# Kernel optimization log

Hardware: AMD Instinct MI355X
Metric: run time of the kernel (lower is better)

The kernel has to match this reference:

```python
import jax, jax.numpy as jnp
import numpy as np

NEG_SLOPE = 0.1  # LeakyReLU alpha from __init__
EPS = 1e-5


def setup_inputs() -> dict:
    key = jax.random.key(0)
    k1, k2, k3, k4, k5 = jax.random.split(key, 5)
    N, E, DIN, DOUT = 10000, 160000, 1024, 1024
    x = jax.random.normal(k1, (N, DIN), dtype=jnp.float32)
    W = jax.random.normal(k2, (DIN, DOUT), dtype=jnp.float32) * 0.02  # xavier-ish gain
    a = jax.random.normal(k3, (1, 2 * DOUT), dtype=jnp.float32) * 0.02
    src = jax.random.randint(k4, (E,), 0, N, dtype=jnp.int64)  # edge rows i
    dst = jax.random.randint(k5, (E,), 0, N, dtype=jnp.int64)  # edge cols j
    return {"x": x, "W": W, "a": a, "src": src, "dst": dst}


def reference(x, W, a, src, dst):
    N = x.shape[0]
    d = W.shape[1]
    h = x @ W                                   # [N, d]
    # a @ cat(h_src, h_dst)^T == (h @ a_l)[src] + (h @ a_r)[dst]
    a_l, a_r = a[0, :d], a[0, d:]
    al = h @ a_l                                # [N]
    ar = h @ a_r                                # [N]
    e = jnp.exp(-jax.nn.leaky_relu(al[src] + ar[dst], negative_slope=NEG_SLOPE))  # [E]
    # sparse rowsum: A @ ones  ->  segment_sum of e over rows
    rowsum = jax.ops.segment_sum(e, src, num_segments=N)          # [N]
    # sparse aggregate: A @ h  (dropout = identity in eval mode)
    h_prime = jax.ops.segment_sum(e[:, None] * h[dst], src, num_segments=N)  # [N, d]
    h_prime = h_prime / (rowsum[:, None] + EPS)
    return jax.nn.elu(h_prime)  # concat=True branch
```

## Files before the change

kernel.cpp:

```cpp
#include <hip/hip_runtime.h>
#include <hip/hip_bf16.h>
#include <stdint.h>
#include <math.h>

#define DK 1024
#define DN 1024
#define CAP 64

typedef __attribute__((ext_vector_type(8))) short bf16x8;
typedef __attribute__((ext_vector_type(4))) float f32x4;

__device__ __forceinline__ unsigned short f2bf(float f) {
  union { float f; uint32_t u; } v; v.f = f;
  uint32_t r = v.u + 0x7FFFu + ((v.u >> 16) & 1u);
  return (unsigned short)(r >> 16);
}
__device__ __forceinline__ float bf2f(unsigned short b) {
  union { uint32_t u; float f; } v; v.u = ((uint32_t)b) << 16; return v.f;
}

__device__ __forceinline__ void gload_lds16(const void* g, void* l) {
  __builtin_amdgcn_global_load_lds((const __attribute__((address_space(1))) unsigned int*)g,
                                   (__attribute__((address_space(3))) unsigned int*)l,
                                   16, 0, 0);
}

__global__ __launch_bounds__(256) void prep_kernel(const float* __restrict__ x,
                                                   unsigned short* __restrict__ xb,
                                                   const float* __restrict__ W,
                                                   unsigned short* __restrict__ Wt,
                                                   int nchunks, int nCast) {
  if ((int)blockIdx.x < nCast) {
    int i = blockIdx.x * 256 + threadIdx.x;
    if (i < nchunks) {
      float4 v = ((const float4*)x)[i];
      ushort4 o;
      o.x = f2bf(v.x); o.y = f2bf(v.y); o.z = f2bf(v.z); o.w = f2bf(v.w);
      ((ushort4*)xb)[i] = o;
    }
  } else {
    __shared__ float t[32][33];
    int bid = blockIdx.x - nCast;
    int tx = threadIdx.x & 31, ty = threadIdx.x >> 5;
    int bk = (bid & 31) * 32, bn = (bid >> 5) * 32;
#pragma unroll
    for (int rr = 0; rr < 4; ++rr) {
      int row = ty + rr * 8;
      t[row][tx] = W[(size_t)(bk + row) * DN + bn + tx];
    }
    __syncthreads();
#pragma unroll
    for (int rr = 0; rr < 4; ++rr) {
      int row = ty + rr * 8;
      Wt[(size_t)(bn + row) * DK + bk + tx] = f2bf(t[tx][row]);
    }
  }
}

__global__ __launch_bounds__(256) void gemm_kernel(const unsigned short* __restrict__ A,
                                                   const unsigned short* __restrict__ Bt,
                                                   unsigned short* __restrict__ Hb,
                                                   int M) {
  __shared__ unsigned short As[128 * 32];
  __shared__ unsigned short Bs[128 * 32];
  const int tid = threadIdx.x;
  const int w = tid >> 6, lane = tid & 63;
  const int r = lane & 15, q = lane >> 4;
  const int m0 = blockIdx.x * 128, n0 = blockIdx.y * 128;
  const int wr = (w >> 1) * 64, wc = (w & 1) * 64;

  const int c0 = w * 64 + lane;
  const int rowA0 = c0 >> 2, g0 = c0 & 3;
  const int rowA1 = rowA0 + 64;
  int gr0 = m0 + rowA0; if (gr0 >= M) gr0 = M - 1;
  int gr1 = m0 + rowA1; if (gr1 >= M) gr1 = M - 1;
  const unsigned short* gA0 = A + (size_t)gr0 * DK + g0 * 8;
  const unsigned short* gA1 = A + (size_t)gr1 * DK + g0 * 8;
  const unsigned short* gB0 = Bt + (size_t)(n0 + rowA0) * DK + g0 * 8;
  const unsigned short* gB1 = Bt + (size_t)(n0 + rowA1) * DK + g0 * 8;
  unsigned short* lA0 = As + w * 512;
  unsigned short* lA1 = As + 2048 + w * 512;
  unsigned short* lB0 = Bs + w * 512;
  unsigned short* lB1 = Bs + 2048 + w * 512;

  const f32x4 zero = {0.f, 0.f, 0.f, 0.f};
  f32x4 acc[4][4];
#pragma unroll
  for (int i = 0; i < 4; ++i)
#pragma unroll
    for (int j = 0; j < 4; ++j) acc[i][j] = zero;

  for (int k0 = 0; k0 < DK; k0 += 32) {
    gload_lds16(gA0, lA0);
    gload_lds16(gA1, lA1);
    gload_lds16(gB0, lB0);
    gload_lds16(gB1, lB1);
    gA0 += 32; gA1 += 32; gB0 += 32; gB1 += 32;
    __syncthreads();

    bf16x8 af[4], bfr[4];
#pragma unroll
    for (int i = 0; i < 4; ++i)
      af[i] = *(const bf16x8*)&As[(wr + i * 16 + r) * 32 + q * 8];
#pragma unroll
    for (int j = 0; j < 4; ++j)
      bfr[j] = *(const bf16x8*)&Bs[(wc + j * 16 + r) * 32 + q * 8];
#pragma unroll
    for (int i = 0; i < 4; ++i)
#pragma unroll
      for (int j = 0; j < 4; ++j)
        acc[i][j] = __builtin_amdgcn_mfma_f32_16x16x32_bf16(af[i], bfr[j], acc[i][j], 0, 0, 0);
    __syncthreads();
  }

#pragma unroll
  for (int i = 0; i < 4; ++i) {
#pragma unroll
    for (int reg = 0; reg < 4; ++reg) {
      int m = m0 + wr + i * 16 + q * 4 + reg;
      if (m < M) {
#pragma unroll
        for (int j = 0; j < 4; ++j) {
          int n = n0 + wc + j * 16 + r;
          Hb[(size_t)m * DN + n] = f2bf(acc[i][j][reg]);
        }
      }
    }
  }
}

__global__ __launch_bounds__(256) void alar_kernel(const unsigned short* __restrict__ Hb,
                                                   const float* __restrict__ a,
                                                   float* __restrict__ al,
                                                   float* __restrict__ ar,
                                                   int M) {
  int row = blockIdx.x;
  int tid = threadIdx.x;
  ushort4 hv = ((const ushort4*)(Hb + (size_t)row * DN))[tid];
  float4 l4 = ((const float4*)a)[tid];
  float4 r4 = ((const float4*)(a + DN))[tid];
  float h0 = bf2f(hv.x), h1 = bf2f(hv.y), h2 = bf2f(hv.z), h3 = bf2f(hv.w);
  float pl = h0 * l4.x + h1 * l4.y + h2 * l4.z + h3 * l4.w;
  float pr = h0 * r4.x + h1 * r4.y + h2 * r4.z + h3 * r4.w;
#pragma unroll
  for (int off = 32; off >= 1; off >>= 1) {
    pl += __shfl_down(pl, off);
    pr += __shfl_down(pr, off);
  }
  __shared__ float sl[4], sr[4];
  int w = tid >> 6, lane = tid & 63;
  if (lane == 0) { sl[w] = pl; sr[w] = pr; }
  __syncthreads();
  if (tid == 0) {
    al[row] = sl[0] + sl[1] + sl[2] + sl[3];
    ar[row] = sr[0] + sr[1] + sr[2] + sr[3];
  }
}

__global__ __launch_bounds__(256) void edge_kernel(const int* __restrict__ src,
                                                   const int* __restrict__ dst,
                                                   const float* __restrict__ al,
                                                   const float* __restrict__ ar,
                                                   int* __restrict__ cnt,
                                                   int* __restrict__ bdst,
                                                   float* __restrict__ be, int E) {
  int i = blockIdx.x * 256 + threadIdx.x;
  if (i < E) {
    int s = src[i], d = dst[i];
    float v = al[s] + ar[d];
    float lr = v > 0.f ? v : 0.1f * v;
    float e = expf(-lr);
    int pos = atomicAdd(&cnt[s], 1);
    if (pos < CAP) {
      bdst[(s << 6) + pos] = d;
      be[(s << 6) + pos] = e;
    }
  }
}

__global__ __launch_bounds__(256) void aggregate_kernel(const int* __restrict__ cnt,
                                                        const int* __restrict__ bdst,
                                                        const float* __restrict__ be,
                                                        const unsigned short* __restrict__ Hb,
                                                        float* __restrict__ out, int M) {
  int row = blockIdx.x;
  int tid = threadIdx.x;
  int n = cnt[row]; if (n > CAP) n = CAP;
  int base = row << 6;
  size_t coff = (size_t)tid * 4;
  float a0 = 0.f, a1 = 0.f, a2 = 0.f, a3 = 0.f, rs = 0.f;
  int p = 0;
  for (; p + 8 <= n; p += 8) {
    int4 da = *(const int4*)(bdst + base + p);
    int4 db = *(const int4*)(bdst + base + p + 4);
    float4 ea = *(const float4*)(be + base + p);
    float4 eb = *(const float4*)(be + base + p + 4);
    ushort4 h0 = *(const ushort4*)&Hb[(size_t)da.x * DN + coff];
    ushort4 h1 = *(const ushort4*)&Hb[(size_t)da.y * DN + coff];
    ushort4 h2 = *(const ushort4*)&Hb[(size_t)da.z * DN + coff];
    ushort4 h3 = *(const ushort4*)&Hb[(size_t)da.w * DN + coff];
    ushort4 h4 = *(const ushort4*)&Hb[(size_t)db.x * DN + coff];
    ushort4 h5 = *(const ushort4*)&Hb[(size_t)db.y * DN + coff];
    ushort4 h6 = *(const ushort4*)&Hb[(size_t)db.z * DN + coff];
    ushort4 h7 = *(const ushort4*)&Hb[(size_t)db.w * DN + coff];
    rs += ((ea.x + ea.y) + (ea.z + ea.w)) + ((eb.x + eb.y) + (eb.z + eb.w));
    a0 += ea.x * bf2f(h0.x) + ea.y * bf2f(h1.x) + ea.z * bf2f(h2.x) + ea.w * bf2f(h3.x)
        + eb.x * bf2f(h4.x) + eb.y * bf2f(h5.x) + eb.z * bf2f(h6.x) + eb.w * bf2f(h7.x);
    a1 += ea.x * bf2f(h0.y) + ea.y * bf2f(h1.y) + ea.z * bf2f(h2.y) + ea.w * bf2f(h3.y)
        + eb.x * bf2f(h4.y) + eb.y * bf2f(h5.y) + eb.z * bf2f(h6.y) + eb.w * bf2f(h7.y);
    a2 += ea.x * bf2f(h0.z) + ea.y * bf2f(h1.z) + ea.z * bf2f(h2.z) + ea.w * bf2f(h3.z)
        + eb.x * bf2f(h4.z) + eb.y * bf2f(h5.z) + eb.z * bf2f(h6.z) + eb.w * bf2f(h7.z);
    a3 += ea.x * bf2f(h0.w) + ea.y * bf2f(h1.w) + ea.z * bf2f(h2.w) + ea.w * bf2f(h3.w)
        + eb.x * bf2f(h4.w) + eb.y * bf2f(h5.w) + eb.z * bf2f(h6.w) + eb.w * bf2f(h7.w);
  }
  for (; p + 4 <= n; p += 4) {
    int4 d4 = *(const int4*)(bdst + base + p);
    float4 e4 = *(const float4*)(be + base + p);
    ushort4 h0 = *(const ushort4*)&Hb[(size_t)d4.x * DN + coff];
    ushort4 h1 = *(const ushort4*)&Hb[(size_t)d4.y * DN + coff];
    ushort4 h2 = *(const ushort4*)&Hb[(size_t)d4.z * DN + coff];
    ushort4 h3 = *(const ushort4*)&Hb[(size_t)d4.w * DN + coff];
    rs += (e4.x + e4.y) + (e4.z + e4.w);
    a0 += e4.x * bf2f(h0.x) + e4.y * bf2f(h1.x) + e4.z * bf2f(h2.x) + e4.w * bf2f(h3.x);
    a1 += e4.x * bf2f(h0.y) + e4.y * bf2f(h1.y) + e4.z * bf2f(h2.y) + e4.w * bf2f(h3.y);
    a2 += e4.x * bf2f(h0.z) + e4.y * bf2f(h1.z) + e4.z * bf2f(h2.z) + e4.w * bf2f(h3.z);
    a3 += e4.x * bf2f(h0.w) + e4.y * bf2f(h1.w) + e4.z * bf2f(h2.w) + e4.w * bf2f(h3.w);
  }
  for (; p < n; ++p) {
    int d = bdst[base + p];
    float e = be[base + p];
    rs += e;
    ushort4 hv = *(const ushort4*)&Hb[(size_t)d * DN + coff];
    a0 += e * bf2f(hv.x);
    a1 += e * bf2f(hv.y);
    a2 += e * bf2f(hv.z);
    a3 += e * bf2f(hv.w);
  }
  float inv = 1.f / (rs + 1e-5f);
  float4 o; float v;
  v = a0 * inv; o.x = v > 0.f ? v : (expf(v) - 1.f);
  v = a1 * inv; o.y = v > 0.f ? v : (expf(v) - 1.f);
  v = a2 * inv; o.z = v > 0.f ? v : (expf(v) - 1.f);
  v = a3 * inv; o.w = v > 0.f ? v : (expf(v) - 1.f);
  ((float4*)(out + (size_t)row * DN))[tid] = o;
}

extern "C" void kernel_launch(void* const* d_in, const int* in_sizes, int n_in,
                              void* d_out, int out_size, void* d_ws, size_t ws_size,
                              hipStream_t stream) {
  const float* x = (const float*)d_in[0];
  const float* W = (const float*)d_in[1];
  const float* a = (const float*)d_in[2];
  const int* src = (const int*)d_in[3];
  const int* dst = (const int*)d_in[4];
  float* out = (float*)d_out;
  const int M = in_sizes[0] / DK;
  const int E = in_sizes[3];

  size_t off = 0;
  auto alloc = [&](size_t bytes) -> void* {
    void* p = (char*)d_ws + off;
    off += (bytes + 255) & ~(size_t)255;
    return p;
  };
  unsigned short* xb   = (unsigned short*)alloc((size_t)M * DK * 2);
  unsigned short* Wt   = (unsigned short*)alloc((size_t)DK * DN * 2);
  unsigned short* Hb   = (unsigned short*)alloc((size_t)M * DN * 2);
  float*          al   = (float*)alloc((size_t)M * 4);
  float*          ar   = (float*)alloc((size_t)M * 4);
  int*            cnt  = (int*)alloc((size_t)M * 4);
  int*            bdst = (int*)alloc((size_t)M * CAP * 4);
  float*          be   = (float*)alloc((size_t)M * CAP * 4);

  hipMemsetAsync(cnt, 0, (size_t)M * 4, stream);

  int nchunks = M * DK / 4;
  int nCast = (nchunks + 255) / 256;
  prep_kernel<<<nCast + (DK / 32) * (DN / 32), 256, 0, stream>>>(x, xb, W, Wt, nchunks, nCast);
  gemm_kernel<<<dim3((M + 127) / 128, DN / 128), 256, 0, stream>>>(xb, Wt, Hb, M);
  alar_kernel<<<M, 256, 0, stream>>>(Hb, a, al, ar, M);
  edge_kernel<<<(E + 255) / 256, 256, 0, stream>>>(src, dst, al, ar, cnt, bdst, be, E);
  aggregate_kernel<<<M, 256, 0, stream>>>(cnt, bdst, be, Hb, out, M);
}
```

Baseline: 201.5 us.

## Compute attention logits via precomputed W·a vectors fused into cast kernel

Result: faster. 194.7 us (-3.4%).

```diff
diff --git a/kernel.cpp b/kernel.cpp
--- a/kernel.cpp
+++ b/kernel.cpp
@@ -25,22 +25,65 @@
                                    16, 0, 0);
 }
 
+__device__ __forceinline__ void block_reduce2(float& pl, float& pr) {
+#pragma unroll
+  for (int off = 32; off >= 1; off >>= 1) {
+    pl += __shfl_down(pl, off);
+    pr += __shfl_down(pr, off);
+  }
+  __shared__ float sl[4], sr[4];
+  int w = threadIdx.x >> 6, lane = threadIdx.x & 63;
+  if (lane == 0) { sl[w] = pl; sr[w] = pr; }
+  __syncthreads();
+  if (threadIdx.x == 0) {
+    pl = sl[0] + sl[1] + sl[2] + sl[3];
+    pr = sr[0] + sr[1] + sr[2] + sr[3];
+  }
+}
+
+__global__ __launch_bounds__(256) void wvec_kernel(const float* __restrict__ W,
+                                                   const float* __restrict__ a,
+                                                   float* __restrict__ wl,
+                                                   float* __restrict__ wr,
+                                                   int* __restrict__ cnt, int M) {
+  int idx = blockIdx.x * 256 + threadIdx.x;
+  if (idx < M) cnt[idx] = 0;
+  int k = blockIdx.x;
+  int tid = threadIdx.x;
+  float4 wv = ((const float4*)(W + (size_t)k * DN))[tid];
+  float4 l4 = ((const float4*)a)[tid];
+  float4 r4 = ((const float4*)(a + DN))[tid];
+  float pl = wv.x * l4.x + wv.y * l4.y + wv.z * l4.z + wv.w * l4.w;
+  float pr = wv.x * r4.x + wv.y * r4.y + wv.z * r4.z + wv.w * r4.w;
+  block_reduce2(pl, pr);
+  if (tid == 0) { wl[k] = pl; wr[k] = pr; }
+}
+
 __global__ __launch_bounds__(256) void prep_kernel(const float* __restrict__ x,
                                                    unsigned short* __restrict__ xb,
                                                    const float* __restrict__ W,
                                                    unsigned short* __restrict__ Wt,
-                                                   int nchunks, int nCast) {
-  if ((int)blockIdx.x < nCast) {
-    int i = blockIdx.x * 256 + threadIdx.x;
-    if (i < nchunks) {
-      float4 v = ((const float4*)x)[i];
-      ushort4 o;
-      o.x = f2bf(v.x); o.y = f2bf(v.y); o.z = f2bf(v.z); o.w = f2bf(v.w);
-      ((ushort4*)xb)[i] = o;
-    }
+                                                   const float* __restrict__ wl,
+                                                   const float* __restrict__ wr,
+                                                   float* __restrict__ al,
+                                                   float* __restrict__ ar,
+                                                   int M) {
+  if ((int)blockIdx.x < M) {
+    int row = blockIdx.x;
+    int tid = threadIdx.x;
+    float4 v = ((const float4*)(x + (size_t)row * DK))[tid];
+    ushort4 o;
+    o.x = f2bf(v.x); o.y = f2bf(v.y); o.z = f2bf(v.z); o.w = f2bf(v.w);
+    ((ushort4*)(xb + (size_t)row * DK))[tid] = o;
+    float4 l4 = ((const float4*)wl)[tid];
+    float4 r4 = ((const float4*)wr)[tid];
+    float pl = v.x * l4.x + v.y * l4.y + v.z * l4.z + v.w * l4.w;
+    float pr = v.x * r4.x + v.y * r4.y + v.z * r4.z + v.w * r4.w;
+    block_reduce2(pl, pr);
+    if (tid == 0) { al[row] = pl; ar[row] = pr; }
   } else {
     __shared__ float t[32][33];
-    int bid = blockIdx.x - nCast;
+    int bid = blockIdx.x - M;
     int tx = threadIdx.x & 31, ty = threadIdx.x >> 5;
     int bk = (bid & 31) * 32, bn = (bid >> 5) * 32;
 #pragma unroll
@@ -126,34 +169,6 @@
         }
       }
     }
-  }
-}
-
-__global__ __launch_bounds__(256) void alar_kernel(const unsigned short* __restrict__ Hb,
-                                                   const float* __restrict__ a,
-                                                   float* __restrict__ al,
-                                                   float* __restrict__ ar,
-                                                   int M) {
-  int row = blockIdx.x;
-  int tid = threadIdx.x;
-  ushort4 hv = ((const ushort4*)(Hb + (size_t)row * DN))[tid];
-  float4 l4 = ((const float4*)a)[tid];
-  float4 r4 = ((const float4*)(a + DN))[tid];
-  float h0 = bf2f(hv.x), h1 = bf2f(hv.y), h2 = bf2f(hv.z), h3 = bf2f(hv.w);
-  float pl = h0 * l4.x + h1 * l4.y + h2 * l4.z + h3 * l4.w;
-  float pr = h0 * r4.x + h1 * r4.y + h2 * r4.z + h3 * r4.w;
-#pragma unroll
-  for (int off = 32; off >= 1; off >>= 1) {
-    pl += __shfl_down(pl, off);
-    pr += __shfl_down(pr, off);
-  }
-  __shared__ float sl[4], sr[4];
-  int w = tid >> 6, lane = tid & 63;
-  if (lane == 0) { sl[w] = pl; sr[w] = pr; }
-  __syncthreads();
-  if (tid == 0) {
-    al[row] = sl[0] + sl[1] + sl[2] + sl[3];
-    ar[row] = sr[0] + sr[1] + sr[2] + sr[3];
   }
 }
 
@@ -268,17 +283,15 @@
   unsigned short* Hb   = (unsigned short*)alloc((size_t)M * DN * 2);
   float*          al   = (float*)alloc((size_t)M * 4);
   float*          ar   = (float*)alloc((size_t)M * 4);
+  float*          wl   = (float*)alloc((size_t)DK * 4);
+  float*          wr   = (float*)alloc((size_t)DK * 4);
   int*            cnt  = (int*)alloc((size_t)M * 4);
   int*            bdst = (int*)alloc((size_t)M * CAP * 4);
   float*          be   = (float*)alloc((size_t)M * CAP * 4);
 
-  hipMemsetAsync(cnt, 0, (size_t)M * 4, stream);
-
-  int nchunks = M * DK / 4;
-  int nCast = (nchunks + 255) / 256;
-  prep_kernel<<<nCast + (DK / 32) * (DN / 32), 256, 0, stream>>>(x, xb, W, Wt, nchunks, nCast);
+  wvec_kernel<<<DK, 256, 0, stream>>>(W, a, wl, wr, cnt, M);
+  prep_kernel<<<M + (DK / 32) * (DN / 32), 256, 0, stream>>>(x, xb, W, Wt, wl, wr, al, ar, M);
   gemm_kernel<<<dim3((M + 127) / 128, DN / 128), 256, 0, stream>>>(xb, Wt, Hb, M);
-  alar_kernel<<<M, 256, 0, stream>>>(Hb, a, al, ar, M);
   edge_kernel<<<(E + 255) / 256, 256, 0, stream>>>(src, dst, al, ar, cnt, bdst, be, E);
   aggregate_kernel<<<M, 256, 0, stream>>>(cnt, bdst, be, Hb, out, M);
 }
```
